# Kernel tuning notes

Measured on AMD Instinct MI355X. Metric: run time of the kernel, lower is better.

The kernel has to match this reference:

```python
import jax, jax.numpy as jnp
import numpy as np

K = 24            # kNN neighbors per DynamicEdgeConv (includes self, dist 0)
N_PER_GRAPH = 128 # uniform nodes per graph
N_GRAPHS = 128
N_IN = 16
HID = 128
N_OUT = 6


def _knn_idx(xg, k):
    # xg: [G, N, D] -> indices of k nearest neighbors per node, [G, N, k]
    sq = jnp.sum(xg * xg, axis=-1)                       # [G, N]
    d2 = sq[:, :, None] + sq[:, None, :] - 2.0 * jnp.einsum('gnd,gmd->gnm', xg, xg)
    _, idx = jax.lax.top_k(-d2, k)                       # smallest distances
    return idx


def _dynamic_edge_conv(xg, w, b, k=K):
    # DynamicEdgeConv: recompute kNN on current features, edge MLP on
    # [x_i, x_j - x_i], max-aggregate over neighbors.
    idx = _knn_idx(xg, k)                                # [G, N, k]
    x_j = jax.vmap(lambda v, i: v[i])(xg, idx)           # [G, N, k, D]
    x_i = xg[:, :, None, :]                              # [G, N, 1, D]
    e = jnp.concatenate([jnp.broadcast_to(x_i, x_j.shape), x_j - x_i], axis=-1)
    h = jax.nn.elu(jnp.einsum('gnkf,fh->gnkh', e, w) + b)
    return jnp.max(h, axis=2)                            # [G, N, H]


def _linear(x, w, b):
    return x @ w + b


def setup_inputs() -> dict:
    key = jax.random.key(0)
    ks = jax.random.split(key, 16)

    def W(k, fi, fo):
        return (jax.random.normal(k, (fi, fo), dtype=jnp.float32) / np.sqrt(fi)).astype(jnp.float32)

    inp = {
        'x_pf': jax.random.normal(ks[0], (N_GRAPHS * N_PER_GRAPH, N_IN), dtype=jnp.float32),
        'enc_w1': W(ks[1], N_IN, HID),  'enc_b1': jnp.zeros((HID,), jnp.float32),
        'enc_w2': W(ks[2], HID, HID),   'enc_b2': jnp.zeros((HID,), jnp.float32),
        'conv1_w': W(ks[3], 2 * HID, HID), 'conv1_b': jnp.zeros((HID,), jnp.float32),
        'conv2_w': W(ks[4], 2 * HID, HID), 'conv2_b': jnp.zeros((HID,), jnp.float32),
        'conv3_w': W(ks[5], 2 * HID, HID), 'conv3_b': jnp.zeros((HID,), jnp.float32),
        'out_w1': W(ks[6], HID, 64), 'out_b1': jnp.zeros((64,), jnp.float32),
        'out_w2': W(ks[7], 64, 32),  'out_b2': jnp.zeros((32,), jnp.float32),
        'out_w3': W(ks[8], 32, 32),  'out_b3': jnp.zeros((32,), jnp.float32),
        'out_w4': W(ks[9], 32, N_OUT), 'out_b4': jnp.zeros((N_OUT,), jnp.float32),
        'batch_pf': jnp.repeat(jnp.arange(N_GRAPHS, dtype=jnp.int64 if jax.config.jax_enable_x64 else jnp.int32), N_PER_GRAPH),
    }
    return inp


def reference(x_pf, enc_w1, enc_b1, enc_w2, enc_b2,
              conv1_w, conv1_b, conv2_w, conv2_b, conv3_w, conv3_b,
              out_w1, out_b1, out_w2, out_b2, out_w3, out_b3, out_w4, out_b4,
              batch_pf):
    G = x_pf.shape[0] // N_PER_GRAPH
    # pf_encode: Linear -> ELU -> Linear -> ELU
    h = jax.nn.elu(_linear(x_pf, enc_w1, enc_b1))
    h = jax.nn.elu(_linear(h, enc_w2, enc_b2))
    hg = h.reshape(G, N_PER_GRAPH, HID)  # uniform graphs; batch_pf = repeat(arange(G))
    hg = _dynamic_edge_conv(hg, conv1_w, conv1_b)
    hg = _dynamic_edge_conv(hg, conv2_w, conv2_b)
    hg = _dynamic_edge_conv(hg, conv3_w, conv3_b)
    # global_add_pool over nodes of each graph
    pooled = jnp.sum(hg, axis=1)                          # [G, HID]
    o = jax.nn.elu(_linear(pooled, out_w1, out_b1))
    o = jax.nn.elu(_linear(o, out_w2, out_b2))
    o = jax.nn.elu(_linear(o, out_w3, out_b3))
    o = _linear(o, out_w4, out_b4)
    return (o, batch_pf)
```

## Files before the change

### kernel.cpp

```cpp
#include <hip/hip_runtime.h>
#include <hip/hip_fp16.h>
#include <hip/hip_bf16.h>
#include <cmath>

#define G_NUM 128
#define NPTS  128
#define FDIM  128
#define KNNK  24
#define NTOT  (G_NUM*NPTS)

typedef short s8v __attribute__((ext_vector_type(8)));
typedef float f32x4 __attribute__((ext_vector_type(4)));

__device__ __forceinline__ float eluf(float x){ return x > 0.0f ? x : expm1f(x); }

__device__ __forceinline__ unsigned short f2bf(float f) {
    unsigned int u = __float_as_uint(f);
    unsigned int r = (u + 0x7fffu + ((u >> 16) & 1u)) >> 16;
    return (unsigned short)r;
}
__device__ __forceinline__ float bf2f(unsigned short b) {
    return __uint_as_float(((unsigned int)b) << 16);
}

__global__ void prep_kernel(const float* __restrict__ w1, const float* __restrict__ w2,
                            const float* __restrict__ w3, const float* __restrict__ ew2,
                            const float* __restrict__ b1, const float* __restrict__ b2,
                            const float* __restrict__ b3,
                            unsigned short* __restrict__ wcatT,
                            unsigned short* __restrict__ enc2T,
                            float* __restrict__ bias,
                            const int* __restrict__ bpf,
                            float* __restrict__ out)
{
    int e = blockIdx.x * 256 + threadIdx.x;
    if (e < 16384) out[768 + e] = (float)bpf[e];
    if (e < 98304) {
        int l = e >> 15;
        int r = e & 32767;
        int k = r >> 8;
        int n = r & 255;
        const float* w = (l == 0) ? w1 : ((l == 1) ? w2 : w3);
        float v = (n < 128) ? (w[k * 128 + n] - w[(128 + k) * 128 + n])
                            : w[(128 + k) * 128 + (n - 128)];
        wcatT[l * 32768 + n * 128 + k] = f2bf(v);
    } else if (e < 114688) {
        int i = e - 98304;
        int k = i >> 7, n = i & 127;
        enc2T[n * 128 + k] = f2bf(ew2[k * 128 + n]);
    } else if (e < 115456) {
        int j = e - 114688;
        int l = j >> 8, c = j & 255;
        const float* b = (l == 0) ? b1 : ((l == 1) ? b2 : b3);
        bias[l * 256 + c] = (c < 128) ? b[c] : 0.0f;
    }
}

#define E_XS  0
#define E_W1  4352
#define E_A   12544
__global__ __launch_bounds__(512) void enc_fused(const float* __restrict__ x_pf,
                                                 const float* __restrict__ w1,
                                                 const float* __restrict__ b1,
                                                 const unsigned short* __restrict__ e2T,
                                                 const float* __restrict__ b2,
                                                 float* __restrict__ hout)
{
    __shared__ char smc[28928];
    float* xs  = (float*)(smc + E_XS);
    float* ws1 = (float*)(smc + E_W1);
    const int tid = threadIdx.x;
    const int m0 = blockIdx.x * 64;

    for (int e = tid; e < 1024; e += 512) {
        int m = e >> 4, k = e & 15;
        xs[m * 17 + k] = x_pf[(size_t)(m0 + m) * 16 + k];
    }
    for (int e = tid; e < 2048; e += 512) ws1[e] = w1[e];
    __syncthreads();

    {
        const int h = tid & 127, mg = tid >> 7;
        float bb = b1[h];
        #pragma unroll
        for (int i = 0; i < 16; ++i) {
            int m = mg * 16 + i;
            float a = bb;
            #pragma unroll
            for (int k = 0; k < 16; ++k) a += xs[m * 17 + k] * ws1[k * 128 + h];
            a = eluf(a);
            int byte = (m * 256 + h * 2) ^ ((m & 15) << 4);
            *reinterpret_cast<unsigned short*>(smc + E_A + byte) = f2bf(a);
        }
    }
    __syncthreads();

    {
        const int l = tid & 63, w = tid >> 6;
        const int lr = l & 15, lg = l >> 4;
        const int mt = w >> 1, nh = w & 1;
        f32x4 acc[4] = {};
        #pragma unroll
        for (int ks = 0; ks < 4; ++ks) {
            int row = mt * 16 + lr;
            int abyte = (row * 256 + ks * 64 + lg * 16) ^ ((row & 15) << 4);
            s8v a_f = *reinterpret_cast<const s8v*>(smc + E_A + abyte);
            #pragma unroll
            for (int ni = 0; ni < 4; ++ni) {
                int n = nh * 64 + ni * 16 + lr;
                s8v b = *reinterpret_cast<const s8v*>(e2T + n * 128 + ks * 32 + lg * 8);
                acc[ni] = __builtin_amdgcn_mfma_f32_16x16x32_bf16(a_f, b, acc[ni], 0, 0, 0);
            }
        }
        #pragma unroll
        for (int ni = 0; ni < 4; ++ni) {
            int n = nh * 64 + ni * 16 + lr;
            float bl = b2[n];
            #pragma unroll
            for (int q = 0; q < 4; ++q)
                hout[(size_t)(m0 + mt * 16 + lg * 4 + q) * 128 + n] = eluf(acc[ni][q] + bl);
        }
    }
}

#define XHI_OFF 0
#define XLO_OFF 32768
#define D_OFF   65536
#define CC_OFF  98816
#define IDX_OFF 132608
#define SQ_OFF  138752
#define CONV_LDS 139264

template<int POOL>
__global__ __launch_bounds__(1024, 4) void conv_fused(const float* __restrict__ hin,
                                                      const unsigned short* __restrict__ wT,
                                                      const float* __restrict__ bias,
                                                      float* __restrict__ hout,
                                                      float* __restrict__ ppool)
{
    extern __shared__ char smc[];
    float* D  = (float*)(smc + D_OFF);
    float* pp = (float*)(smc + D_OFF);
    float* Sq = (float*)(smc + SQ_OFF);
    unsigned int* idxL = (unsigned int*)(smc + IDX_OFF);
    unsigned int* Cc   = (unsigned int*)(smc + CC_OFF);

    const int bid = blockIdx.x;
    const int g  = (bid & 7) * 16 + (bid >> 4);
    const int hf = (bid >> 3) & 1;
    const int r0 = hf * 64;
    const int tid = threadIdx.x;
    const float* hg = hin + (size_t)g * NPTS * FDIM;
    float* og = hout + (size_t)g * NPTS * FDIM;

    {
        const int m = tid >> 3;
        const int k0 = (tid & 7) * 16;
        float sq = 0.f;
        #pragma unroll
        for (int i = 0; i < 4; ++i) {
            float4 v = *reinterpret_cast<const float4*>(&hg[m * 128 + k0 + 4 * i]);
            ushort4 hi, lo;
            hi.x = f2bf(v.x); lo.x = f2bf(v.x - bf2f(hi.x));
            hi.y = f2bf(v.y); lo.y = f2bf(v.y - bf2f(hi.y));
            hi.z = f2bf(v.z); lo.z = f2bf(v.z - bf2f(hi.z));
            hi.w = f2bf(v.w); lo.w = f2bf(v.w - bf2f(hi.w));
            sq += v.x * v.x + v.y * v.y + v.z * v.z + v.w * v.w;
            int byte = (m * 256 + (k0 + 4 * i) * 2) ^ ((m & 15) << 4);
            *reinterpret_cast<ushort4*>(smc + XHI_OFF + byte) = hi;
            *reinterpret_cast<ushort4*>(smc + XLO_OFF + byte) = lo;
        }
        sq += __shfl_xor(sq, 1);
        sq += __shfl_xor(sq, 2);
        sq += __shfl_xor(sq, 4);
        if ((tid & 7) == 0) Sq[m] = sq;
    }
    __syncthreads();

    const int l = tid & 63, w = tid >> 6;
    const int lr = l & 15, lg = l >> 4;

    if (w < 8) {
        const int t2 = w >> 1;
        const int nh = w & 1;
        const int arow = r0 + t2 * 16 + lr;
        const int aswz = (arow & 15) << 4;
        f32x4 acc[4] = {};
        #pragma unroll
        for (int ks = 0; ks < 4; ++ks) {
            int abyte = (arow * 256 + ks * 64 + lg * 16) ^ aswz;
            s8v ahi = *reinterpret_cast<const s8v*>(smc + XHI_OFF + abyte);
            s8v alo = *reinterpret_cast<const s8v*>(smc + XLO_OFF + abyte);
            #pragma unroll
            for (int ni = 0; ni < 4; ++ni) {
                int brow = (nh * 4 + ni) * 16 + lr;
                int bbyte = (brow * 256 + ks * 64 + lg * 16) ^ ((brow & 15) << 4);
                s8v bhi = *reinterpret_cast<const s8v*>(smc + XHI_OFF + bbyte);
                s8v blo = *reinterpret_cast<const s8v*>(smc + XLO_OFF + bbyte);
                acc[ni] = __builtin_amdgcn_mfma_f32_16x16x32_bf16(alo, bhi, acc[ni], 0, 0, 0);
                acc[ni] = __builtin_amdgcn_mfma_f32_16x16x32_bf16(ahi, blo, acc[ni], 0, 0, 0);
                acc[ni] = __builtin_amdgcn_mfma_f32_16x16x32_bf16(ahi, bhi, acc[ni], 0, 0, 0);
            }
        }
        float sqa[4];
        #pragma unroll
        for (int q = 0; q < 4; ++q) sqa[q] = Sq[r0 + t2 * 16 + lg * 4 + q];
        #pragma unroll
        for (int ni = 0; ni < 4; ++ni) {
            int col = (nh * 4 + ni) * 16 + lr;
            float sqc = Sq[col];
            #pragma unroll
            for (int q = 0; q < 4; ++q)
                D[(t2 * 16 + lg * 4 + q) * 130 + col] = sqa[q] + sqc - 2.f * acc[ni][q];
        }
    } else {
        const int jt = w - 8;
        f32x4 acc[8] = {};
        #pragma unroll
        for (int ks = 0; ks < 4; ++ks) {
            int row = jt * 16 + lr;
            int byte = (row * 256 + ks * 64 + lg * 16) ^ ((row & 15) << 4);
            s8v a_f = *reinterpret_cast<const s8v*>(smc + XHI_OFF + byte);
            #pragma unroll
            for (int ni = 0; ni < 8; ++ni) {
                int n = 128 + ni * 16 + lr;
                s8v b = *reinterpret_cast<const s8v*>(wT + n * 128 + ks * 32 + lg * 8);
                acc[ni] = __builtin_amdgcn_mfma_f32_16x16x32_bf16(a_f, b, acc[ni], 0, 0, 0);
            }
        }
        #pragma unroll
        for (int ni = 0; ni < 8; ++ni)
            #pragma unroll
            for (int q = 0; q < 4; ++q) {
                float v = acc[ni][q];
                float p = __shfl_xor(v, 1);
                if (!(lr & 1)) {
                    unsigned int u =
                        ((unsigned int)__half_as_ushort(__float2half(p)) << 16)
                      |  (unsigned int)__half_as_ushort(__float2half(v));
                    int j = jt * 16 + lg * 4 + q;
                    Cc[j * 66 + ni * 8 + (lr >> 1)] = u;
                }
            }
    }
    __syncthreads();

    {
        const int mt = w >> 2;
        const int nb = (w & 3) * 2;
        const int arow = r0 + mt * 16 + lr;
        const int aswz = (arow & 15) << 4;
        f32x4 acc[2] = {};
        #pragma unroll
        for (int ks = 0; ks < 4; ++ks) {
            int abyte = (arow * 256 + ks * 64 + lg * 16) ^ aswz;
            s8v a_f = *reinterpret_cast<const s8v*>(smc + XHI_OFF + abyte);
            #pragma unroll
            for (int ni = 0; ni < 2; ++ni) {
                int n = (nb + ni) * 16 + lr;
                s8v b = *reinterpret_cast<const s8v*>(wT + n * 128 + ks * 32 + lg * 8);
                acc[ni] = __builtin_amdgcn_mfma_f32_16x16x32_bf16(a_f, b, acc[ni], 0, 0, 0);
            }
        }
        #pragma unroll
        for (int ni = 0; ni < 2; ++ni) {
            int h = (nb + ni) * 16 + lr;
            float bl = bias[h];
            #pragma unroll
            for (int q = 0; q < 4; ++q) {
                int row = mt * 16 + lg * 4 + q;
                int byte = (row * 512 + h * 4) ^ ((row & 3) << 4);
                *reinterpret_cast<float*>(smc + XLO_OFF + byte) = acc[ni][q] + bl;
            }
        }
    }

    for (int lr2 = w * 4; lr2 < w * 4 + 4; ++lr2) {
        float2 cur = *reinterpret_cast<const float2*>(&D[lr2 * 130 + 2 * l]);
        unsigned int ub0 = __float_as_uint(cur.x);
        unsigned int ub1 = __float_as_uint(cur.y);
        unsigned int u0 = (ub0 & 0x80000000u) ? ~ub0 : (ub0 | 0x80000000u);
        unsigned int u1 = (ub1 & 0x80000000u) ? ~ub1 : (ub1 | 0x80000000u);

        bool c0 = true, c1 = true, in0 = false, in1 = false;
        int need = KNNK;
        for (int b = 31; b >= 0; --b) {
            bool z0 = c0 && !((u0 >> b) & 1u);
            bool z1 = c1 && !((u1 >> b) & 1u);
            int cnt = __popcll(__ballot(z0)) + __popcll(__ballot(z1));
            if (cnt > need) { c0 = z0; c1 = z1; }
            else if (cnt == need) { in0 |= z0; in1 |= z1; need = 0; break; }
            else { in0 |= z0; in1 |= z1; need -= cnt;
                   c0 = c0 && !z0; c1 = c1 && !z1; }
        }
        if (need > 0) {
            unsigned long long m0 = __ballot(c0), m1 = __ballot(c1);
            unsigned long long below = (1ull << l) - 1ull;
            int rk0 = __popcll(m0 & below) + __popcll(m1 & below);
            int rk1 = rk0 + (int)((m0 >> l) & 1ull);
            in0 = in0 || (c0 && rk0 < need);
            in1 = in1 || (c1 && rk1 < need);
        }
        unsigned long long f0 = __ballot(in0), f1 = __ballot(in1);
        int cnt0 = __popcll(f0);
        unsigned long long below = (1ull << l) - 1ull;
        if (in0) idxL[lr2 * KNNK + __popcll(f0 & below)] = 2 * l;
        if (in1) idxL[lr2 * KNNK + cnt0 + __popcll(f1 & below)] = 2 * l + 1;
    }
    __syncthreads();

    {
        const int hh = l >> 5, jl = l & 31;
        float4 ps = {0.f, 0.f, 0.f, 0.f};
        #pragma unroll
        for (int u = 0; u < 2; ++u) {
            const int r = w * 4 + 2 * u + hh;
            const unsigned int* il = &idxL[r * KNNK];
            float mc0 = -3.0e38f, mc1 = -3.0e38f, mc2 = -3.0e38f, mc3 = -3.0e38f;
            #pragma unroll
            for (int t = 0; t < KNNK; t += 4) {
                unsigned int p0 = il[t], p1 = il[t + 1], p2 = il[t + 2], p3 = il[t + 3];
                uint2 a = *reinterpret_cast<const uint2*>(&Cc[p0 * 66 + 2 * jl]);
                uint2 b = *reinterpret_cast<const uint2*>(&Cc[p1 * 66 + 2 * jl]);
                uint2 c = *reinterpret_cast<const uint2*>(&Cc[p2 * 66 + 2 * jl]);
                uint2 d = *reinterpret_cast<const uint2*>(&Cc[p3 * 66 + 2 * jl]);
                mc0 = fmaxf(fmaxf(mc0,
                        __half2float(__ushort_as_half((unsigned short)(a.x & 0xffffu)))),
                        fmaxf(__half2float(__ushort_as_half((unsigned short)(b.x & 0xffffu))),
                              fmaxf(__half2float(__ushort_as_half((unsigned short)(c.x & 0xffffu))),
                                    __half2float(__ushort_as_half((unsigned short)(d.x & 0xffffu))))));
                mc1 = fmaxf(fmaxf(mc1,
                        __half2float(__ushort_as_half((unsigned short)(a.x >> 16)))),
                        fmaxf(__half2float(__ushort_as_half((unsigned short)(b.x >> 16))),
                              fmaxf(__half2float(__ushort_as_half((unsigned short)(c.x >> 16))),
                                    __half2float(__ushort_as_half((unsigned short)(d.x >> 16))))));
                mc2 = fmaxf(fmaxf(mc2,
                        __half2float(__ushort_as_half((unsigned short)(a.y & 0xffffu)))),
                        fmaxf(__half2float(__ushort_as_half((unsigned short)(b.y & 0xffffu))),
                              fmaxf(__half2float(__ushort_as_half((unsigned short)(c.y & 0xffffu))),
                                    __half2float(__ushort_as_half((unsigned short)(d.y & 0xffffu))))));
                mc3 = fmaxf(fmaxf(mc3,
                        __half2float(__ushort_as_half((unsigned short)(a.y >> 16)))),
                        fmaxf(__half2float(__ushort_as_half((unsigned short)(b.y >> 16))),
                              fmaxf(__half2float(__ushort_as_half((unsigned short)(c.y >> 16))),
                                    __half2float(__ushort_as_half((unsigned short)(d.y >> 16))))));
            }
            int abyte = (r * 512 + 16 * jl) ^ ((r & 3) << 4);
            float4 av = *reinterpret_cast<const float4*>(smc + XLO_OFF + abyte);
            float4 o;
            o.x = eluf(av.x + mc0);
            o.y = eluf(av.y + mc1);
            o.z = eluf(av.z + mc2);
            o.w = eluf(av.w + mc3);
            if (!POOL) {
                *reinterpret_cast<float4*>(&og[(r0 + r) * 128 + 4 * jl]) = o;
            } else {
                ps.x += o.x; ps.y += o.y; ps.z += o.z; ps.w += o.w;
            }
        }
        if (POOL) {
            *reinterpret_cast<float4*>(&pp[(w * 2 + hh) * 132 + 4 * jl]) = ps;
            __syncthreads();
            if (tid < 128) {
                float s = 0.f;
                #pragma unroll 8
                for (int rg = 0; rg < 32; ++rg) s += pp[rg * 132 + tid];
                ppool[(g * 2 + hf) * 128 + tid] = s;
            }
        }
    }
}

__global__ __launch_bounds__(128) void head_kernel(const float* __restrict__ ppool,
        const float* __restrict__ w1, const float* __restrict__ b1,
        const float* __restrict__ w2, const float* __restrict__ b2,
        const float* __restrict__ w3, const float* __restrict__ b3,
        const float* __restrict__ w4, const float* __restrict__ b4,
        float* __restrict__ out)
{
    __shared__ float pooled[128], s1[64], s2[32], s3[32];
    const int g = blockIdx.x, t = threadIdx.x;
    pooled[t] = ppool[(2 * g) * 128 + t] + ppool[(2 * g + 1) * 128 + t];
    __syncthreads();
    if (t < 64) {
        float a = b1[t];
        #pragma unroll 8
        for (int k = 0; k < 128; ++k) a += pooled[k] * w1[k * 64 + t];
        s1[t] = eluf(a);
    }
    __syncthreads();
    if (t < 32) {
        float a = b2[t];
        #pragma unroll 8
        for (int k = 0; k < 64; ++k) a += s1[k] * w2[k * 32 + t];
        s2[t] = eluf(a);
    }
    __syncthreads();
    if (t < 32) {
        float a = b3[t];
        #pragma unroll 8
        for (int k = 0; k < 32; ++k) a += s2[k] * w3[k * 32 + t];
        s3[t] = eluf(a);
    }
    __syncthreads();
    if (t < 6) {
        float a = b4[t];
        #pragma unroll 8
        for (int k = 0; k < 32; ++k) a += s3[k] * w4[k * 6 + t];
        out[g * 6 + t] = a;
    }
}

extern "C" void kernel_launch(void* const* d_in, const int* in_sizes, int n_in,
                              void* d_out, int out_size, void* d_ws, size_t ws_size,
                              hipStream_t stream)
{
    const float* x_pf   = (const float*)d_in[0];
    const float* enc_w1 = (const float*)d_in[1];
    const float* enc_b1 = (const float*)d_in[2];
    const float* enc_w2 = (const float*)d_in[3];
    const float* enc_b2 = (const float*)d_in[4];
    const float* c1w = (const float*)d_in[5];
    const float* c1b = (const float*)d_in[6];
    const float* c2w = (const float*)d_in[7];
    const float* c2b = (const float*)d_in[8];
    const float* c3w = (const float*)d_in[9];
    const float* c3b = (const float*)d_in[10];
    const float* o_w1 = (const float*)d_in[11];
    const float* o_b1 = (const float*)d_in[12];
    const float* o_w2 = (const float*)d_in[13];
    const float* o_b2 = (const float*)d_in[14];
    const float* o_w3 = (const float*)d_in[15];
    const float* o_b3 = (const float*)d_in[16];
    const float* o_w4 = (const float*)d_in[17];
    const float* o_b4 = (const float*)d_in[18];
    const int*   bpf  = (const int*)d_in[19];
    float* out = (float*)d_out;

    float* ws   = (float*)d_ws;
    float* h_a  = ws;
    float* h_b  = h_a + (size_t)NTOT * FDIM;
    float* ppool = h_b + (size_t)NTOT * FDIM;
    unsigned short* wcatT = (unsigned short*)(ppool + 256 * 128);
    unsigned short* enc2T = wcatT + 3 * 32768;
    float* biasF = (float*)(enc2T + 16384);

    prep_kernel<<<451, 256, 0, stream>>>(c1w, c2w, c3w, enc_w2,
                                         c1b, c2b, c3b, wcatT, enc2T, biasF,
                                         bpf, out);

    enc_fused<<<NTOT / 64, 512, 0, stream>>>(x_pf, enc_w1, enc_b1,
                                             enc2T, enc_b2, h_a);

    conv_fused<0><<<2 * G_NUM, 1024, CONV_LDS, stream>>>(
        h_a, wcatT, biasF, h_b, ppool);
    conv_fused<0><<<2 * G_NUM, 1024, CONV_LDS, stream>>>(
        h_b, wcatT + 32768, biasF + 256, h_a, ppool);
    conv_fused<1><<<2 * G_NUM, 1024, CONV_LDS, stream>>>(
        h_a, wcatT + 65536, biasF + 512, h_b, ppool);

    head_kernel<<<G_NUM, 128, 0, stream>>>(ppool, o_w1, o_b1, o_w2, o_b2,
                                           o_w3, o_b3, o_w4, o_b4, out);
}
```

Before: 257.9 us.

## Split edge-conv linear GEMMs into separate kernel and shrink per-graph conv blocks

Moves the per-node A/C projections (x·W_top + b and x·W_bottom) out of the fused conv kernel into a standalone tiled MFMA GEMM over all nodes. The result goes to global buffers: A in fp32, C packed as fp16 pairs. The conv kernel now only computes the distance matrix, top-k and gather-max, and uses 512-thread blocks over quarter-graphs (4 blocks per graph) with about half the LDS and byte indices. The aim is to remove the redundant per-half recomputation of C and to raise occupancy and parallelism. In exchange it adds an extra launch per layer and an extra global round trip for A and C, and the neighbour gathers now read from global/L2 instead of LDS.

```diff
diff --git a/kernel.cpp b/kernel.cpp
--- a/kernel.cpp
+++ b/kernel.cpp
@@ -123,42 +123,133 @@
     }
 }
 
-#define XHI_OFF 0
-#define XLO_OFF 32768
-#define D_OFF   65536
-#define CC_OFF  98816
-#define IDX_OFF 132608
-#define SQ_OFF  138752
-#define CONV_LDS 139264
-
-template<int POOL>
-__global__ __launch_bounds__(1024, 4) void conv_fused(const float* __restrict__ hin,
-                                                      const unsigned short* __restrict__ wT,
-                                                      const float* __restrict__ bias,
-                                                      float* __restrict__ hout,
-                                                      float* __restrict__ ppool)
+__global__ __launch_bounds__(256) void cgemm(const float* __restrict__ A,
+                                             const unsigned short* __restrict__ Bt,
+                                             const float* __restrict__ bias,
+                                             float* __restrict__ a_out,
+                                             unsigned int* __restrict__ c16)
 {
     extern __shared__ char smc[];
-    float* D  = (float*)(smc + D_OFF);
-    float* pp = (float*)(smc + D_OFF);
-    float* Sq = (float*)(smc + SQ_OFF);
-    unsigned int* idxL = (unsigned int*)(smc + IDX_OFF);
-    unsigned int* Cc   = (unsigned int*)(smc + CC_OFF);
+    const int tid = threadIdx.x;
+    const int m0 = blockIdx.x * 128;
+    const unsigned short* Btg = Bt + (size_t)blockIdx.y * 16384;
+
+    for (int e = tid; e < 4096; e += 256) {
+        int m = e >> 5, q = e & 31;
+        float4 v = *reinterpret_cast<const float4*>(&A[(size_t)(m0 + m) * 128 + 4 * q]);
+        ushort4 p;
+        p.x = f2bf(v.x); p.y = f2bf(v.y); p.z = f2bf(v.z); p.w = f2bf(v.w);
+        int byte = (m * 256 + q * 8) ^ ((m & 15) << 4);
+        *reinterpret_cast<ushort4*>(smc + byte) = p;
+    }
+    for (int e = tid; e < 2048; e += 256) {
+        int n = e >> 4, q = e & 15;
+        uint4 v = *reinterpret_cast<const uint4*>(Btg + n * 128 + q * 8);
+        int byte = (n * 256 + q * 16) ^ ((n & 15) << 4);
+        *reinterpret_cast<uint4*>(smc + 32768 + byte) = v;
+    }
+    __syncthreads();
+
+    const int l = tid & 63, w = tid >> 6;
+    const int wr = w >> 1, wc = w & 1;
+    const int lr = l & 15, lg = l >> 4;
+
+    f32x4 acc[4][4] = {};
+    #pragma unroll
+    for (int ks = 0; ks < 4; ++ks) {
+        s8v a_f[4], b_f[4];
+        #pragma unroll
+        for (int mi = 0; mi < 4; ++mi) {
+            int row = wr * 64 + mi * 16 + lr;
+            int byte = (row * 256 + ks * 64 + lg * 16) ^ ((row & 15) << 4);
+            a_f[mi] = *reinterpret_cast<const s8v*>(smc + byte);
+        }
+        #pragma unroll
+        for (int ni = 0; ni < 4; ++ni) {
+            int n = wc * 64 + ni * 16 + lr;
+            int byte = (n * 256 + ks * 64 + lg * 16) ^ ((n & 15) << 4);
+            b_f[ni] = *reinterpret_cast<const s8v*>(smc + 32768 + byte);
+        }
+        #pragma unroll
+        for (int mi = 0; mi < 4; ++mi)
+            #pragma unroll
+            for (int ni = 0; ni < 4; ++ni)
+                acc[mi][ni] = __builtin_amdgcn_mfma_f32_16x16x32_bf16(
+                    a_f[mi], b_f[ni], acc[mi][ni], 0, 0, 0);
+    }
+
+    if (blockIdx.y == 0) {
+        float bl[4];
+        #pragma unroll
+        for (int ni = 0; ni < 4; ++ni) bl[ni] = bias[wc * 64 + ni * 16 + lr];
+        #pragma unroll
+        for (int mi = 0; mi < 4; ++mi) {
+            int rbase = m0 + wr * 64 + mi * 16 + lg * 4;
+            #pragma unroll
+            for (int ni = 0; ni < 4; ++ni) {
+                int col = wc * 64 + ni * 16 + lr;
+                #pragma unroll
+                for (int q = 0; q < 4; ++q)
+                    a_out[(size_t)(rbase + q) * 128 + col] = acc[mi][ni][q] + bl[ni];
+            }
+        }
+    } else {
+        #pragma unroll
+        for (int mi = 0; mi < 4; ++mi) {
+            int rbase = m0 + wr * 64 + mi * 16 + lg * 4;
+            #pragma unroll
+            for (int ni = 0; ni < 4; ++ni) {
+                int col = wc * 64 + ni * 16 + lr;
+                #pragma unroll
+                for (int q = 0; q < 4; ++q) {
+                    float v = acc[mi][ni][q];
+                    float p = __shfl_xor(v, 1);
+                    if (!(lr & 1)) {
+                        unsigned int u =
+                            ((unsigned int)__half_as_ushort(__float2half(p)) << 16)
+                          |  (unsigned int)__half_as_ushort(__float2half(v));
+                        c16[(size_t)(rbase + q) * 64 + (col >> 1)] = u;
+                    }
+                }
+            }
+        }
+    }
+}
+
+#define CV_XHI 0
+#define CV_XLO 32768
+#define CV_D   32768
+#define CV_PP  (32768 + 16384)
+#define CV_IDX (32768 + 24576)
+#define CV_SQ  65536
+#define CONV_LDS 66048
+
+template<int POOL>
+__global__ __launch_bounds__(512, 4) void conv_fused(const float* __restrict__ hin,
+                                                     const float* __restrict__ a_buf,
+                                                     const unsigned int* __restrict__ c16,
+                                                     float* __restrict__ hout,
+                                                     float* __restrict__ ppool)
+{
+    extern __shared__ char smc[];
+    float* Sq = (float*)(smc + CV_SQ);
+    unsigned char* idxL = (unsigned char*)(smc + CV_IDX);
+    float* pp = (float*)(smc + CV_PP);
 
     const int bid = blockIdx.x;
-    const int g  = (bid & 7) * 16 + (bid >> 4);
-    const int hf = (bid >> 3) & 1;
-    const int r0 = hf * 64;
+    const int g   = (bid & 7) * 16 + (bid >> 5);
+    const int sub = (bid >> 3) & 3;
+    const int r0  = sub * 32;
     const int tid = threadIdx.x;
     const float* hg = hin + (size_t)g * NPTS * FDIM;
     float* og = hout + (size_t)g * NPTS * FDIM;
 
     {
-        const int m = tid >> 3;
-        const int k0 = (tid & 7) * 16;
+        const int m = tid >> 2;
+        const int k0 = (tid & 3) * 32;
         float sq = 0.f;
         #pragma unroll
-        for (int i = 0; i < 4; ++i) {
+        for (int i = 0; i < 8; ++i) {
             float4 v = *reinterpret_cast<const float4*>(&hg[m * 128 + k0 + 4 * i]);
             ushort4 hi, lo;
             hi.x = f2bf(v.x); lo.x = f2bf(v.x - bf2f(hi.x));
@@ -167,116 +258,60 @@
             hi.w = f2bf(v.w); lo.w = f2bf(v.w - bf2f(hi.w));
             sq += v.x * v.x + v.y * v.y + v.z * v.z + v.w * v.w;
             int byte = (m * 256 + (k0 + 4 * i) * 2) ^ ((m & 15) << 4);
-            *reinterpret_cast<ushort4*>(smc + XHI_OFF + byte) = hi;
-            *reinterpret_cast<ushort4*>(smc + XLO_OFF + byte) = lo;
+            *reinterpret_cast<ushort4*>(smc + CV_XHI + byte) = hi;
+            *reinterpret_cast<ushort4*>(smc + CV_XLO + byte) = lo;
         }
         sq += __shfl_xor(sq, 1);
         sq += __shfl_xor(sq, 2);
-        sq += __shfl_xor(sq, 4);
-        if ((tid & 7) == 0) Sq[m] = sq;
+        if ((tid & 3) == 0) Sq[m] = sq;
     }
     __syncthreads();
 
     const int l = tid & 63, w = tid >> 6;
     const int lr = l & 15, lg = l >> 4;
 
-    if (w < 8) {
-        const int t2 = w >> 1;
-        const int nh = w & 1;
-        const int arow = r0 + t2 * 16 + lr;
-        const int aswz = (arow & 15) << 4;
-        f32x4 acc[4] = {};
-        #pragma unroll
-        for (int ks = 0; ks < 4; ++ks) {
-            int abyte = (arow * 256 + ks * 64 + lg * 16) ^ aswz;
-            s8v ahi = *reinterpret_cast<const s8v*>(smc + XHI_OFF + abyte);
-            s8v alo = *reinterpret_cast<const s8v*>(smc + XLO_OFF + abyte);
-            #pragma unroll
-            for (int ni = 0; ni < 4; ++ni) {
-                int brow = (nh * 4 + ni) * 16 + lr;
-                int bbyte = (brow * 256 + ks * 64 + lg * 16) ^ ((brow & 15) << 4);
-                s8v bhi = *reinterpret_cast<const s8v*>(smc + XHI_OFF + bbyte);
-                s8v blo = *reinterpret_cast<const s8v*>(smc + XLO_OFF + bbyte);
-                acc[ni] = __builtin_amdgcn_mfma_f32_16x16x32_bf16(alo, bhi, acc[ni], 0, 0, 0);
-                acc[ni] = __builtin_amdgcn_mfma_f32_16x16x32_bf16(ahi, blo, acc[ni], 0, 0, 0);
-                acc[ni] = __builtin_amdgcn_mfma_f32_16x16x32_bf16(ahi, bhi, acc[ni], 0, 0, 0);
-            }
-        }
-        float sqa[4];
-        #pragma unroll
-        for (int q = 0; q < 4; ++q) sqa[q] = Sq[r0 + t2 * 16 + lg * 4 + q];
-        #pragma unroll
-        for (int ni = 0; ni < 4; ++ni) {
-            int col = (nh * 4 + ni) * 16 + lr;
-            float sqc = Sq[col];
-            #pragma unroll
-            for (int q = 0; q < 4; ++q)
-                D[(t2 * 16 + lg * 4 + q) * 130 + col] = sqa[q] + sqc - 2.f * acc[ni][q];
-        }
-    } else {
-        const int jt = w - 8;
-        f32x4 acc[8] = {};
-        #pragma unroll
-        for (int ks = 0; ks < 4; ++ks) {
-            int row = jt * 16 + lr;
-            int byte = (row * 256 + ks * 64 + lg * 16) ^ ((row & 15) << 4);
-            s8v a_f = *reinterpret_cast<const s8v*>(smc + XHI_OFF + byte);
-            #pragma unroll
-            for (int ni = 0; ni < 8; ++ni) {
-                int n = 128 + ni * 16 + lr;
-                s8v b = *reinterpret_cast<const s8v*>(wT + n * 128 + ks * 32 + lg * 8);
-                acc[ni] = __builtin_amdgcn_mfma_f32_16x16x32_bf16(a_f, b, acc[ni], 0, 0, 0);
-            }
-        }
-        #pragma unroll
-        for (int ni = 0; ni < 8; ++ni)
-            #pragma unroll
-            for (int q = 0; q < 4; ++q) {
-                float v = acc[ni][q];
-                float p = __shfl_xor(v, 1);
-                if (!(lr & 1)) {
-                    unsigned int u =
-                        ((unsigned int)__half_as_ushort(__float2half(p)) << 16)
-                      |  (unsigned int)__half_as_ushort(__float2half(v));
-                    int j = jt * 16 + lg * 4 + q;
-                    Cc[j * 66 + ni * 8 + (lr >> 1)] = u;
-                }
-            }
-    }
-    __syncthreads();
-
-    {
-        const int mt = w >> 2;
-        const int nb = (w & 3) * 2;
-        const int arow = r0 + mt * 16 + lr;
-        const int aswz = (arow & 15) << 4;
-        f32x4 acc[2] = {};
-        #pragma unroll
-        for (int ks = 0; ks < 4; ++ks) {
-            int abyte = (arow * 256 + ks * 64 + lg * 16) ^ aswz;
-            s8v a_f = *reinterpret_cast<const s8v*>(smc + XHI_OFF + abyte);
-            #pragma unroll
-            for (int ni = 0; ni < 2; ++ni) {
-                int n = (nb + ni) * 16 + lr;
-                s8v b = *reinterpret_cast<const s8v*>(wT + n * 128 + ks * 32 + lg * 8);
-                acc[ni] = __builtin_amdgcn_mfma_f32_16x16x32_bf16(a_f, b, acc[ni], 0, 0, 0);
-            }
-        }
-        #pragma unroll
-        for (int ni = 0; ni < 2; ++ni) {
-            int h = (nb + ni) * 16 + lr;
-            float bl = bias[h];
-            #pragma unroll
-            for (int q = 0; q < 4; ++q) {
-                int row = mt * 16 + lg * 4 + q;
-                int byte = (row * 512 + h * 4) ^ ((row & 3) << 4);
-                *reinterpret_cast<float*>(smc + XLO_OFF + byte) = acc[ni][q] + bl;
-            }
-        }
-    }
-
-    for (int lr2 = w * 4; lr2 < w * 4 + 4; ++lr2) {
-        float2 cur = *reinterpret_cast<const float2*>(&D[lr2 * 130 + 2 * l]);
+    f32x4 acc[2] = {};
+    const int rt = w & 1, ct0 = w >> 1;
+    const int arow = r0 + rt * 16 + lr;
+    const int aswz = (arow & 15) << 4;
+    #pragma unroll
+    for (int ks = 0; ks < 4; ++ks) {
+        int abyte = (arow * 256 + ks * 64 + lg * 16) ^ aswz;
+        s8v ahi = *reinterpret_cast<const s8v*>(smc + CV_XHI + abyte);
+        s8v alo = *reinterpret_cast<const s8v*>(smc + CV_XLO + abyte);
+        #pragma unroll
+        for (int t = 0; t < 2; ++t) {
+            int brow = (ct0 + 4 * t) * 16 + lr;
+            int bbyte = (brow * 256 + ks * 64 + lg * 16) ^ ((brow & 15) << 4);
+            s8v bhi = *reinterpret_cast<const s8v*>(smc + CV_XHI + bbyte);
+            s8v blo = *reinterpret_cast<const s8v*>(smc + CV_XLO + bbyte);
+            acc[t] = __builtin_amdgcn_mfma_f32_16x16x32_bf16(alo, bhi, acc[t], 0, 0, 0);
+            acc[t] = __builtin_amdgcn_mfma_f32_16x16x32_bf16(ahi, blo, acc[t], 0, 0, 0);
+            acc[t] = __builtin_amdgcn_mfma_f32_16x16x32_bf16(ahi, bhi, acc[t], 0, 0, 0);
+        }
+    }
+    float sqa[4], sqc[2];
+    #pragma unroll
+    for (int q = 0; q < 4; ++q) sqa[q] = Sq[r0 + rt * 16 + lg * 4 + q];
+    #pragma unroll
+    for (int t = 0; t < 2; ++t) sqc[t] = Sq[(ct0 + 4 * t) * 16 + lr];
+    __syncthreads();
+
+    #pragma unroll
+    for (int t = 0; t < 2; ++t) {
+        int col = (ct0 + 4 * t) * 16 + lr;
+        #pragma unroll
+        for (int q = 0; q < 4; ++q) {
+            int row = rt * 16 + lg * 4 + q;
+            *reinterpret_cast<float*>(smc + CV_D + ((row * 512 + col * 4) ^ ((row & 7) << 4)))
+                = sqa[q] + sqc[t] - 2.f * acc[t][q];
+        }
+    }
+    __syncthreads();
+
+    for (int r = w * 4; r < w * 4 + 4; ++r) {
+        float2 cur = *reinterpret_cast<const float2*>(
+            smc + CV_D + ((r * 512 + 8 * l) ^ ((r & 7) << 4)));
         unsigned int ub0 = __float_as_uint(cur.x);
         unsigned int ub1 = __float_as_uint(cur.y);
         unsigned int u0 = (ub0 & 0x80000000u) ? ~ub0 : (ub0 | 0x80000000u);
@@ -304,26 +339,28 @@
         unsigned long long f0 = __ballot(in0), f1 = __ballot(in1);
         int cnt0 = __popcll(f0);
         unsigned long long below = (1ull << l) - 1ull;
-        if (in0) idxL[lr2 * KNNK + __popcll(f0 & below)] = 2 * l;
-        if (in1) idxL[lr2 * KNNK + cnt0 + __popcll(f1 & below)] = 2 * l + 1;
-    }
-    __syncthreads();
+        if (in0) idxL[r * KNNK + __popcll(f0 & below)] = (unsigned char)(2 * l);
+        if (in1) idxL[r * KNNK + cnt0 + __popcll(f1 & below)] = (unsigned char)(2 * l + 1);
+    }
 
     {
         const int hh = l >> 5, jl = l & 31;
+        const float* ag = a_buf + ((size_t)g * 128 + r0) * 128;
+        const unsigned int* cg = c16 + (size_t)g * 128 * 64;
         float4 ps = {0.f, 0.f, 0.f, 0.f};
         #pragma unroll
         for (int u = 0; u < 2; ++u) {
             const int r = w * 4 + 2 * u + hh;
-            const unsigned int* il = &idxL[r * KNNK];
+            const unsigned char* il = &idxL[r * KNNK];
+            float4 av = *reinterpret_cast<const float4*>(&ag[r * 128 + 4 * jl]);
             float mc0 = -3.0e38f, mc1 = -3.0e38f, mc2 = -3.0e38f, mc3 = -3.0e38f;
             #pragma unroll
             for (int t = 0; t < KNNK; t += 4) {
-                unsigned int p0 = il[t], p1 = il[t + 1], p2 = il[t + 2], p3 = il[t + 3];
-                uint2 a = *reinterpret_cast<const uint2*>(&Cc[p0 * 66 + 2 * jl]);
-                uint2 b = *reinterpret_cast<const uint2*>(&Cc[p1 * 66 + 2 * jl]);
-                uint2 c = *reinterpret_cast<const uint2*>(&Cc[p2 * 66 + 2 * jl]);
-                uint2 d = *reinterpret_cast<const uint2*>(&Cc[p3 * 66 + 2 * jl]);
+                int p0 = il[t], p1 = il[t + 1], p2 = il[t + 2], p3 = il[t + 3];
+                uint2 a = *reinterpret_cast<const uint2*>(&cg[(size_t)p0 * 64 + 2 * jl]);
+                uint2 b = *reinterpret_cast<const uint2*>(&cg[(size_t)p1 * 64 + 2 * jl]);
+                uint2 c = *reinterpret_cast<const uint2*>(&cg[(size_t)p2 * 64 + 2 * jl]);
+                uint2 d = *reinterpret_cast<const uint2*>(&cg[(size_t)p3 * 64 + 2 * jl]);
                 mc0 = fmaxf(fmaxf(mc0,
                         __half2float(__ushort_as_half((unsigned short)(a.x & 0xffffu)))),
                         fmaxf(__half2float(__ushort_as_half((unsigned short)(b.x & 0xffffu))),
@@ -345,8 +382,6 @@
                               fmaxf(__half2float(__ushort_as_half((unsigned short)(c.y >> 16))),
                                     __half2float(__ushort_as_half((unsigned short)(d.y >> 16))))));
             }
-            int abyte = (r * 512 + 16 * jl) ^ ((r & 3) << 4);
-            float4 av = *reinterpret_cast<const float4*>(smc + XLO_OFF + abyte);
             float4 o;
             o.x = eluf(av.x + mc0);
             o.y = eluf(av.y + mc1);
@@ -359,13 +394,13 @@
             }
         }
         if (POOL) {
-            *reinterpret_cast<float4*>(&pp[(w * 2 + hh) * 132 + 4 * jl]) = ps;
+            *reinterpret_cast<float4*>(&pp[(w * 2 + hh) * 128 + 4 * jl]) = ps;
             __syncthreads();
             if (tid < 128) {
                 float s = 0.f;
                 #pragma unroll 8
-                for (int rg = 0; rg < 32; ++rg) s += pp[rg * 132 + tid];
-                ppool[(g * 2 + hf) * 128 + tid] = s;
+                for (int rg = 0; rg < 16; ++rg) s += pp[rg * 128 + tid];
+                ppool[(size_t)(g * 4 + sub) * 128 + tid] = s;
             }
         }
     }
@@ -380,7 +415,8 @@
 {
     __shared__ float pooled[128], s1[64], s2[32], s3[32];
     const int g = blockIdx.x, t = threadIdx.x;
-    pooled[t] = ppool[(2 * g) * 128 + t] + ppool[(2 * g + 1) * 128 + t];
+    pooled[t] = ppool[(size_t)(4 * g) * 128 + t] + ppool[(size_t)(4 * g + 1) * 128 + t]
+              + ppool[(size_t)(4 * g + 2) * 128 + t] + ppool[(size_t)(4 * g + 3) * 128 + t];
     __syncthreads();
     if (t < 64) {
         float a = b1[t];
@@ -437,11 +473,13 @@
     const int*   bpf  = (const int*)d_in[19];
     float* out = (float*)d_out;
 
-    float* ws   = (float*)d_ws;
-    float* h_a  = ws;
-    float* h_b  = h_a + (size_t)NTOT * FDIM;
-    float* ppool = h_b + (size_t)NTOT * FDIM;
-    unsigned short* wcatT = (unsigned short*)(ppool + 256 * 128);
+    float* ws    = (float*)d_ws;
+    float* h_a   = ws;
+    float* h_b   = h_a + (size_t)NTOT * FDIM;
+    float* a_buf = h_b + (size_t)NTOT * FDIM;
+    unsigned int* c16 = (unsigned int*)(a_buf + (size_t)NTOT * FDIM);
+    float* ppool = (float*)(c16 + (size_t)NTOT * 64);
+    unsigned short* wcatT = (unsigned short*)(ppool + 512 * 128);
     unsigned short* enc2T = wcatT + 3 * 32768;
     float* biasF = (float*)(enc2T + 16384);
 
@@ -452,12 +490,17 @@
     enc_fused<<<NTOT / 64, 512, 0, stream>>>(x_pf, enc_w1, enc_b1,
                                              enc2T, enc_b2, h_a);
 
-    conv_fused<0><<<2 * G_NUM, 1024, CONV_LDS, stream>>>(
-        h_a, wcatT, biasF, h_b, ppool);
-    conv_fused<0><<<2 * G_NUM, 1024, CONV_LDS, stream>>>(
-        h_b, wcatT + 32768, biasF + 256, h_a, ppool);
-    conv_fused<1><<<2 * G_NUM, 1024, CONV_LDS, stream>>>(
-        h_a, wcatT + 65536, biasF + 512, h_b, ppool);
+    float* hc = h_a;
+    float* hn = h_b;
+    for (int lyr = 0; lyr < 3; ++lyr) {
+        cgemm<<<dim3(NTOT / 128, 2), 256, 65536, stream>>>(
+            hc, wcatT + (size_t)lyr * 32768, biasF + lyr * 256, a_buf, c16);
+        if (lyr < 2)
+            conv_fused<0><<<512, 512, CONV_LDS, stream>>>(hc, a_buf, c16, hn, ppool);
+        else
+            conv_fused<1><<<512, 512, CONV_LDS, stream>>>(hc, a_buf, c16, hn, ppool);
+        float* t = hc; hc = hn; hn = t;
+    }
 
     head_kernel<<<G_NUM, 128, 0, stream>>>(ppool, o_w1, o_b1, o_w2, o_b2,
                                            o_w3, o_b3, o_w4, o_b4, out);
```

Measured after the change: 265.7 us. 3.0% more time.
